# Optimization experiments

Hardware: AMD Instinct MI355X
Metric: run time of the kernel (lower is better)

## Reference

```python
import jax, jax.numpy as jnp
import numpy as np

WH, WW = 8, 8
DIM, HEADS = 256, 8
HEAD_DIM = DIM // HEADS
N = WH * WW  # 64 tokens per window
B = 2048     # total windows = real_batch * windows_per_image
MASK_NW = 64 # windows per image


def _relative_position_index():
    coords = np.stack(np.meshgrid(np.arange(WH), np.arange(WW), indexing='ij'))  # [2,WH,WW]
    flat = coords.reshape(2, -1)                         # [2,N]
    rel = flat[:, :, None] - flat[:, None, :]            # [2,N,N]
    rel = rel.transpose(1, 2, 0)                         # [N,N,2]
    rel[:, :, 0] += WH - 1
    rel[:, :, 1] += WW - 1
    rel[:, :, 0] *= 2 * WW - 1
    return jnp.asarray(rel.sum(-1), dtype=jnp.int32)     # [N,N]


def setup_inputs() -> dict:
    key = jax.random.key(0)
    ks = jax.random.split(key, 10)
    s = 0.02
    return {
        'hidden_states': jax.random.normal(ks[0], (B, N, DIM), jnp.float32),
        'attention_mask': jax.random.normal(ks[1], (MASK_NW, N, N), jnp.float32),
        'wq': jax.random.normal(ks[2], (DIM, DIM), jnp.float32) * s,
        'bq': jax.random.normal(ks[3], (DIM,), jnp.float32) * s,
        'wk': jax.random.normal(ks[4], (DIM, DIM), jnp.float32) * s,
        'bk': jax.random.normal(ks[5], (DIM,), jnp.float32) * s,
        'wv': jax.random.normal(ks[6], (DIM, DIM), jnp.float32) * s,
        'bv': jax.random.normal(ks[7], (DIM,), jnp.float32) * s,
        'bias_table': jax.random.normal(ks[8], ((2 * WH - 1) * (2 * WW - 1), HEADS), jnp.float32) * s,
        'rel_index': _relative_position_index(),
    }


def reference(hidden_states, attention_mask, wq, bq, wk, bk, wv, bv, bias_table, rel_index):
    batch, n, _ = hidden_states.shape
    def heads(x):  # [B,N,D] -> [B,H,N,hd]
        return x.reshape(batch, n, HEADS, HEAD_DIM).transpose(0, 2, 1, 3)
    q = heads(hidden_states @ wq.T + bq)
    k = heads(hidden_states @ wk.T + bk)
    v = heads(hidden_states @ wv.T + bv)
    scores = jnp.einsum('bhqd,bhkd->bhqk', q, k) / jnp.sqrt(jnp.float32(HEAD_DIM))
    # gathered relative position bias: [N,N,H] -> [H,N,N]
    rel_bias = bias_table[rel_index].transpose(2, 0, 1)
    scores = scores + rel_bias[None]
    # shifted-window mask: scores [B//nW, nW, H, N, N] + mask [nW,1? ...]
    nW = attention_mask.shape[0]
    scores = scores.reshape(batch // nW, nW, HEADS, n, n) + attention_mask[None, :, None]
    scores = scores.reshape(batch, HEADS, n, n)
    probs = jax.nn.softmax(scores, axis=-1)
    ctx = jnp.einsum('bhqk,bhkd->bhqd', probs, v)
    ctx = ctx.transpose(0, 2, 1, 3).reshape(batch, n, DIM)
    return ctx
```

## Files before the change

### kernel.cpp

```cpp
#include <hip/hip_runtime.h>

#define TOK 64
#define DIMS 256
#define NHEAD 8
#define HDIM 32

typedef __attribute__((ext_vector_type(8))) short short8;
typedef __attribute__((ext_vector_type(4))) float floatx4;
typedef __attribute__((ext_vector_type(2))) unsigned int uintx2;

__device__ __forceinline__ unsigned short f2bf(float f) {
  unsigned int u = __float_as_uint(f);
  u += 0x7fffu + ((u >> 16) & 1u);
  return (unsigned short)(u >> 16);
}

__global__ void prep_w(const float* __restrict__ wq, const float* __restrict__ bq,
                       const float* __restrict__ wk, const float* __restrict__ bk,
                       const float* __restrict__ wv, const float* __restrict__ bv,
                       const float* __restrict__ bias_table, const int* __restrict__ rel_index,
                       unsigned short* __restrict__ Wqkv, float* __restrict__ bias,
                       float* __restrict__ rbT) {
  const int o = blockIdx.x;
  const int t = threadIdx.x;
  const float scale = 0.17677669529663687f;
  const float* src; float s;
  if (o < 256)      { src = wq + o * 256;         s = scale; }
  else if (o < 512) { src = wk + (o - 256) * 256; s = 1.0f; }
  else              { src = wv + (o - 512) * 256; s = 1.0f; }
  Wqkv[o * 256 + t] = f2bf(src[t] * s);
  if (o == 0)      bias[t]       = bq[t] * scale;
  else if (o == 1) bias[256 + t] = bk[t];
  else if (o == 2) bias[512 + t] = bv[t];
  if (o < 128) {
    int idx = o * 256 + t;
    int h = idx >> 12, j = (idx >> 6) & 63, i = idx & 63;
    rbT[idx] = bias_table[rel_index[i * 64 + j] * 8 + h];
  }
}

__global__ void prep_mask(const float* __restrict__ mask, float* __restrict__ maskT) {
  int idx = blockIdx.x * 256 + threadIdx.x;
  int w = idx >> 12, j = (idx >> 6) & 63, i = idx & 63;
  maskT[idx] = mask[(w << 12) + (i << 6) + j];
}

__global__ __launch_bounds__(256, 1)
void attn_fused(const float* __restrict__ hidden, const unsigned short* __restrict__ Wqkv,
                const float* __restrict__ bias, const float* __restrict__ rbT,
                const float* __restrict__ maskT, float* __restrict__ out) {
  __shared__ unsigned short sAP[18432];
  __shared__ unsigned short sQ[18432];
  __shared__ unsigned short sK[18432];
  __shared__ unsigned short sV[18432];

  const int b    = blockIdx.x;
  const int t    = threadIdx.x;
  const int wave = t >> 6;
  const int lane = t & 63;
  const int quad = lane >> 4;
  const int l16  = lane & 15;

  {
    const float* hsrc = hidden + (size_t)b * (TOK * DIMS);
    #pragma unroll
    for (int it = 0; it < 16; ++it) {
      int e = (it * 256 + t) * 4;
      int row = e >> 8, col = e & 255;
      floatx4 v = *(const floatx4*)(hsrc + e);
      union { unsigned short s[4]; uintx2 u; } pk;
      pk.s[0] = f2bf(v.x); pk.s[1] = f2bf(v.y);
      pk.s[2] = f2bf(v.z); pk.s[3] = f2bf(v.w);
      *(uintx2*)&sAP[row * 264 + col] = pk.u;
    }
  }
  __syncthreads();

  {
    const int colw = wave * 192;
    #pragma unroll 1
    for (int pass = 0; pass < 2; ++pass) {
      const int pbase = colw + pass * 96;
      floatx4 acc[6][4];
      #pragma unroll
      for (int nt = 0; nt < 6; ++nt)
        #pragma unroll
        for (int mt = 0; mt < 4; ++mt)
          acc[nt][mt] = (floatx4){0.f, 0.f, 0.f, 0.f};
      #pragma unroll
      for (int kk = 0; kk < 8; ++kk) {
        const int koff = kk * 32 + quad * 8;
        short8 af[4];
        #pragma unroll
        for (int mt = 0; mt < 4; ++mt)
          af[mt] = *(const short8*)&sAP[(mt * 16 + l16) * 264 + koff];
        #pragma unroll
        for (int nt = 0; nt < 6; ++nt) {
          const short8 wf = *(const short8*)(Wqkv + (pbase + nt * 16 + l16) * 256 + koff);
          #pragma unroll
          for (int mt = 0; mt < 4; ++mt)
            acc[nt][mt] = __builtin_amdgcn_mfma_f32_16x16x32_bf16(af[mt], wf, acc[nt][mt], 0, 0, 0);
        }
      }
      #pragma unroll
      for (int nt = 0; nt < 6; ++nt) {
        const int col = pbase + nt * 16 + l16;
        const float bo = bias[col];
        const int region = col >> 8;
        const int head = (col >> 5) & 7;
        const int c = col & 31;
        #pragma unroll
        for (int mt = 0; mt < 4; ++mt) {
          const int row0 = mt * 16 + quad * 4;
          if (region == 2) {
            union { unsigned short s[4]; uintx2 u; } pk;
            #pragma unroll
            for (int r = 0; r < 4; ++r) pk.s[r] = f2bf(acc[nt][mt][r] + bo);
            *(uintx2*)&sV[(head * 32 + c) * 72 + row0] = pk.u;
          } else {
            unsigned short* dst = (region == 0 ? sQ : sK) + (head * 64 + row0) * 36 + c;
            #pragma unroll
            for (int r = 0; r < 4; ++r) dst[r * 36] = f2bf(acc[nt][mt][r] + bo);
          }
        }
      }
    }
  }
  __syncthreads();

  const int wmod = b & 63;
  const float* mw = maskT + wmod * 4096;
  unsigned short* sP = sAP + wave * (64 * 72);

  #pragma unroll 1
  for (int rep = 0; rep < 2; ++rep) {
    const int h = wave * 2 + rep;
    floatx4 sacc[4][4];
    #pragma unroll
    for (int mt = 0; mt < 4; ++mt)
      #pragma unroll
      for (int nt = 0; nt < 4; ++nt)
        sacc[mt][nt] = (floatx4){0.f, 0.f, 0.f, 0.f};
    short8 qf[4];
    #pragma unroll
    for (int mt = 0; mt < 4; ++mt) {
      const unsigned short* qp = sQ + (h * 64 + mt * 16 + l16) * 36 + quad * 8;
      union { short8 s8; uintx2 u2[2]; } u;
      u.u2[0] = *(const uintx2*)qp;
      u.u2[1] = *(const uintx2*)(qp + 4);
      qf[mt] = u.s8;
    }
    #pragma unroll
    for (int nt = 0; nt < 4; ++nt) {
      const unsigned short* kp = sK + (h * 64 + nt * 16 + l16) * 36 + quad * 8;
      union { short8 s8; uintx2 u2[2]; } u;
      u.u2[0] = *(const uintx2*)kp;
      u.u2[1] = *(const uintx2*)(kp + 4);
      const short8 kf = u.s8;
      #pragma unroll
      for (int mt = 0; mt < 4; ++mt)
        sacc[mt][nt] = __builtin_amdgcn_mfma_f32_16x16x32_bf16(qf[mt], kf, sacc[mt][nt], 0, 0, 0);
    }
    const float* rb = rbT + h * 4096;
    #pragma unroll
    for (int mt = 0; mt < 4; ++mt) {
      const int i0 = mt * 16 + quad * 4;
      #pragma unroll
      for (int nt = 0; nt < 4; ++nt) {
        const int j = nt * 16 + l16;
        floatx4 rv = *(const floatx4*)(rb + j * 64 + i0);
        floatx4 mv = *(const floatx4*)(mw + j * 64 + i0);
        sacc[mt][nt] += rv + mv;
      }
    }
    #pragma unroll
    for (int mt = 0; mt < 4; ++mt) {
      #pragma unroll
      for (int r = 0; r < 4; ++r) {
        float v0 = sacc[mt][0][r], v1 = sacc[mt][1][r];
        float v2 = sacc[mt][2][r], v3 = sacc[mt][3][r];
        float mx = fmaxf(fmaxf(v0, v1), fmaxf(v2, v3));
        mx = fmaxf(mx, __shfl_xor(mx, 1));
        mx = fmaxf(mx, __shfl_xor(mx, 2));
        mx = fmaxf(mx, __shfl_xor(mx, 4));
        mx = fmaxf(mx, __shfl_xor(mx, 8));
        float e0 = __expf(v0 - mx), e1 = __expf(v1 - mx);
        float e2 = __expf(v2 - mx), e3 = __expf(v3 - mx);
        float sm = (e0 + e1) + (e2 + e3);
        sm += __shfl_xor(sm, 1);
        sm += __shfl_xor(sm, 2);
        sm += __shfl_xor(sm, 4);
        sm += __shfl_xor(sm, 8);
        const float inv = __builtin_amdgcn_rcpf(sm);
        sacc[mt][0][r] = e0 * inv; sacc[mt][1][r] = e1 * inv;
        sacc[mt][2][r] = e2 * inv; sacc[mt][3][r] = e3 * inv;
      }
    }
    #pragma unroll
    for (int mt = 0; mt < 4; ++mt) {
      const int i0 = mt * 16 + quad * 4;
      #pragma unroll
      for (int nt = 0; nt < 4; ++nt) {
        const int j = nt * 16 + l16;
        #pragma unroll
        for (int r = 0; r < 4; ++r)
          sP[(i0 + r) * 72 + j] = f2bf(sacc[mt][nt][r]);
      }
    }
    __syncthreads();
    floatx4 cacc[4][2];
    #pragma unroll
    for (int mt = 0; mt < 4; ++mt) {
      cacc[mt][0] = (floatx4){0.f, 0.f, 0.f, 0.f};
      cacc[mt][1] = (floatx4){0.f, 0.f, 0.f, 0.f};
    }
    #pragma unroll
    for (int kk = 0; kk < 2; ++kk) {
      const int joff = kk * 32 + quad * 8;
      short8 pf[4];
      #pragma unroll
      for (int mt = 0; mt < 4; ++mt)
        pf[mt] = *(const short8*)&sP[(mt * 16 + l16) * 72 + joff];
      #pragma unroll
      for (int dt = 0; dt < 2; ++dt) {
        const short8 vf = *(const short8*)&sV[(h * 32 + dt * 16 + l16) * 72 + joff];
        #pragma unroll
        for (int mt = 0; mt < 4; ++mt)
          cacc[mt][dt] = __builtin_amdgcn_mfma_f32_16x16x32_bf16(pf[mt], vf, cacc[mt][dt], 0, 0, 0);
      }
    }
    float* ob = out + (size_t)b * (TOK * DIMS) + h * 32;
    #pragma unroll
    for (int mt = 0; mt < 4; ++mt) {
      const int i0 = mt * 16 + quad * 4;
      #pragma unroll
      for (int dt = 0; dt < 2; ++dt) {
        #pragma unroll
        for (int r = 0; r < 4; ++r)
          ob[(i0 + r) * 256 + dt * 16 + l16] = cacc[mt][dt][r];
      }
    }
  }
}

extern "C" void kernel_launch(void* const* d_in, const int* in_sizes, int n_in,
                              void* d_out, int out_size, void* d_ws, size_t ws_size,
                              hipStream_t stream) {
  const float* hidden = (const float*)d_in[0];
  const float* mask   = (const float*)d_in[1];
  const float* wq = (const float*)d_in[2];
  const float* bq = (const float*)d_in[3];
  const float* wk = (const float*)d_in[4];
  const float* bk = (const float*)d_in[5];
  const float* wv = (const float*)d_in[6];
  const float* bv = (const float*)d_in[7];
  const float* bias_table = (const float*)d_in[8];
  const int*   rel_index  = (const int*)d_in[9];

  char* ws = (char*)d_ws;
  unsigned short* Wqkv = (unsigned short*)ws;
  float* bias  = (float*)(ws + 393216);
  float* rbT   = (float*)(ws + 393216 + 3072);
  float* maskT = (float*)(ws + 393216 + 3072 + 131072);

  prep_w<<<768, 256, 0, stream>>>(wq, bq, wk, bk, wv, bv, bias_table, rel_index,
                                  Wqkv, bias, rbT);
  prep_mask<<<1024, 256, 0, stream>>>(mask, maskT);
  attn_fused<<<2048, 256, 0, stream>>>(hidden, Wqkv, bias, rbT, maskT, (float*)d_out);
}
```

Before: 472.8 us.

## Compute QKV per head inside attention loop to shrink LDS and double occupancy

Restructures the fused kernel so each wave projects Q, K and V only for the head it is about to attend, keeping per-wave Q/K/V/P buffers instead of full-window QKV in shared memory. LDS use drops from about 144KB to 80KB and launch bounds move to 2 blocks per CU, so more blocks can be resident. Padded layouts are replaced by XOR-swizzled layouts so fragments load as single 16-byte reads without bank conflicts. It adds an extra barrier per head iteration and reloads hidden-state fragments for each head, and the register cap from 2-block occupancy may cause spills.

```diff
diff --git a/kernel.cpp b/kernel.cpp
--- a/kernel.cpp
+++ b/kernel.cpp
@@ -45,14 +45,11 @@
   maskT[idx] = mask[(w << 12) + (i << 6) + j];
 }
 
-__global__ __launch_bounds__(256, 1)
+__global__ __launch_bounds__(256, 2)
 void attn_fused(const float* __restrict__ hidden, const unsigned short* __restrict__ Wqkv,
                 const float* __restrict__ bias, const float* __restrict__ rbT,
                 const float* __restrict__ maskT, float* __restrict__ out) {
-  __shared__ unsigned short sAP[18432];
-  __shared__ unsigned short sQ[18432];
-  __shared__ unsigned short sK[18432];
-  __shared__ unsigned short sV[18432];
+  __shared__ __align__(16) unsigned short smem[40960];
 
   const int b    = blockIdx.x;
   const int t    = threadIdx.x;
@@ -60,6 +57,12 @@
   const int lane = t & 63;
   const int quad = lane >> 4;
   const int l16  = lane & 15;
+
+  unsigned short* sA = smem;
+  unsigned short* sQ = smem + 16384 + wave * 6144;
+  unsigned short* sK = sQ + 2048;
+  unsigned short* sV = sK + 2048;
+  unsigned short* sP = sQ;
 
   {
     const float* hsrc = hidden + (size_t)b * (TOK * DIMS);
@@ -71,32 +74,37 @@
       union { unsigned short s[4]; uintx2 u; } pk;
       pk.s[0] = f2bf(v.x); pk.s[1] = f2bf(v.y);
       pk.s[2] = f2bf(v.z); pk.s[3] = f2bf(v.w);
-      *(uintx2*)&sAP[row * 264 + col] = pk.u;
+      *(uintx2*)&sA[row * 256 + (col ^ ((row & 7) << 3))] = pk.u;
     }
   }
   __syncthreads();
 
-  {
-    const int colw = wave * 192;
-    #pragma unroll 1
-    for (int pass = 0; pass < 2; ++pass) {
-      const int pbase = colw + pass * 96;
+  const int wmod = b & 63;
+  const float* mw = maskT + wmod * 4096;
+
+  #pragma unroll 1
+  for (int rep = 0; rep < 2; ++rep) {
+    const int h = wave * 2 + rep;
+
+    {
       floatx4 acc[6][4];
       #pragma unroll
       for (int nt = 0; nt < 6; ++nt)
         #pragma unroll
         for (int mt = 0; mt < 4; ++mt)
           acc[nt][mt] = (floatx4){0.f, 0.f, 0.f, 0.f};
+      const int aswz = (l16 & 7) << 3;
       #pragma unroll
       for (int kk = 0; kk < 8; ++kk) {
         const int koff = kk * 32 + quad * 8;
         short8 af[4];
         #pragma unroll
         for (int mt = 0; mt < 4; ++mt)
-          af[mt] = *(const short8*)&sAP[(mt * 16 + l16) * 264 + koff];
+          af[mt] = *(const short8*)&sA[(mt * 16 + l16) * 256 + (koff ^ aswz)];
         #pragma unroll
         for (int nt = 0; nt < 6; ++nt) {
-          const short8 wf = *(const short8*)(Wqkv + (pbase + nt * 16 + l16) * 256 + koff);
+          const int wrow = (nt >> 1) * 256 + h * 32 + (nt & 1) * 16 + l16;
+          const short8 wf = *(const short8*)(Wqkv + wrow * 256 + koff);
           #pragma unroll
           for (int mt = 0; mt < 4; ++mt)
             acc[nt][mt] = __builtin_amdgcn_mfma_f32_16x16x32_bf16(af[mt], wf, acc[nt][mt], 0, 0, 0);
@@ -104,11 +112,9 @@
       }
       #pragma unroll
       for (int nt = 0; nt < 6; ++nt) {
-        const int col = pbase + nt * 16 + l16;
-        const float bo = bias[col];
-        const int region = col >> 8;
-        const int head = (col >> 5) & 7;
-        const int c = col & 31;
+        const int region = nt >> 1;
+        const int fc = (nt & 1) * 16 + l16;
+        const float bo = bias[region * 256 + h * 32 + fc];
         #pragma unroll
         for (int mt = 0; mt < 4; ++mt) {
           const int row0 = mt * 16 + quad * 4;
@@ -116,25 +122,20 @@
             union { unsigned short s[4]; uintx2 u; } pk;
             #pragma unroll
             for (int r = 0; r < 4; ++r) pk.s[r] = f2bf(acc[nt][mt][r] + bo);
-            *(uintx2*)&sV[(head * 32 + c) * 72 + row0] = pk.u;
+            *(uintx2*)&sV[fc * 64 + (row0 ^ ((fc & 7) << 3))] = pk.u;
           } else {
-            unsigned short* dst = (region == 0 ? sQ : sK) + (head * 64 + row0) * 36 + c;
+            unsigned short* dst = region ? sK : sQ;
             #pragma unroll
-            for (int r = 0; r < 4; ++r) dst[r * 36] = f2bf(acc[nt][mt][r] + bo);
+            for (int r = 0; r < 4; ++r) {
+              const int row = row0 + r;
+              dst[row * 32 + (fc ^ (((row >> 1) & 3) << 3))] = f2bf(acc[nt][mt][r] + bo);
+            }
           }
         }
       }
     }
-  }
-  __syncthreads();
-
-  const int wmod = b & 63;
-  const float* mw = maskT + wmod * 4096;
-  unsigned short* sP = sAP + wave * (64 * 72);
-
-  #pragma unroll 1
-  for (int rep = 0; rep < 2; ++rep) {
-    const int h = wave * 2 + rep;
+    __syncthreads();
+
     floatx4 sacc[4][4];
     #pragma unroll
     for (int mt = 0; mt < 4; ++mt)
@@ -144,19 +145,13 @@
     short8 qf[4];
     #pragma unroll
     for (int mt = 0; mt < 4; ++mt) {
-      const unsigned short* qp = sQ + (h * 64 + mt * 16 + l16) * 36 + quad * 8;
-      union { short8 s8; uintx2 u2[2]; } u;
-      u.u2[0] = *(const uintx2*)qp;
-      u.u2[1] = *(const uintx2*)(qp + 4);
-      qf[mt] = u.s8;
+      const int tok = mt * 16 + l16;
+      qf[mt] = *(const short8*)&sQ[tok * 32 + ((quad * 8) ^ (((tok >> 1) & 3) << 3))];
     }
     #pragma unroll
     for (int nt = 0; nt < 4; ++nt) {
-      const unsigned short* kp = sK + (h * 64 + nt * 16 + l16) * 36 + quad * 8;
-      union { short8 s8; uintx2 u2[2]; } u;
-      u.u2[0] = *(const uintx2*)kp;
-      u.u2[1] = *(const uintx2*)(kp + 4);
-      const short8 kf = u.s8;
+      const int tok = nt * 16 + l16;
+      const short8 kf = *(const short8*)&sK[tok * 32 + ((quad * 8) ^ (((tok >> 1) & 3) << 3))];
       #pragma unroll
       for (int mt = 0; mt < 4; ++mt)
         sacc[mt][nt] = __builtin_amdgcn_mfma_f32_16x16x32_bf16(qf[mt], kf, sacc[mt][nt], 0, 0, 0);
@@ -203,11 +198,14 @@
       for (int nt = 0; nt < 4; ++nt) {
         const int j = nt * 16 + l16;
         #pragma unroll
-        for (int r = 0; r < 4; ++r)
-          sP[(i0 + r) * 72 + j] = f2bf(sacc[mt][nt][r]);
+        for (int r = 0; r < 4; ++r) {
+          const int i = i0 + r;
+          sP[i * 64 + (j ^ ((i & 7) << 3))] = f2bf(sacc[mt][nt][r]);
+        }
       }
     }
     __syncthreads();
+
     floatx4 cacc[4][2];
     #pragma unroll
     for (int mt = 0; mt < 4; ++mt) {
@@ -219,11 +217,14 @@
       const int joff = kk * 32 + quad * 8;
       short8 pf[4];
       #pragma unroll
-      for (int mt = 0; mt < 4; ++mt)
-        pf[mt] = *(const short8*)&sP[(mt * 16 + l16) * 72 + joff];
+      for (int mt = 0; mt < 4; ++mt) {
+        const int i = mt * 16 + l16;
+        pf[mt] = *(const short8*)&sP[i * 64 + (joff ^ ((i & 7) << 3))];
+      }
       #pragma unroll
       for (int dt = 0; dt < 2; ++dt) {
-        const short8 vf = *(const short8*)&sV[(h * 32 + dt * 16 + l16) * 72 + joff];
+        const int feat = dt * 16 + l16;
+        const short8 vf = *(const short8*)&sV[feat * 64 + (joff ^ ((feat & 7) << 3))];
         #pragma unroll
         for (int mt = 0; mt < 4; ++mt)
           cacc[mt][dt] = __builtin_amdgcn_mfma_f32_16x16x32_bf16(pf[mt], vf, cacc[mt][dt], 0, 0, 0);
@@ -240,6 +241,7 @@
           ob[(i0 + r) * 256 + dt * 16 + l16] = cacc[mt][dt][r];
       }
     }
+    __syncthreads();
   }
 }
 
```

Result: slower. 628.0 us (+32.8%).
